# Optimization experiments

Hardware: AMD Instinct MI355X
Metric: run time of the kernel (lower is better)

## Reference

```python
import jax, jax.numpy as jnp
import numpy as np

HIDDEN = 1024
FFN = 4096
NUM_EXPERTS = 8
TOKENS = 4096


def setup_inputs() -> dict:
    key = jax.random.key(0)
    k1, k2, k3, k4 = jax.random.split(key, 4)
    x = jax.random.normal(k1, (TOKENS, HIDDEN), dtype=jnp.float32)
    router_weight = jax.random.normal(k2, (HIDDEN, NUM_EXPERTS), dtype=jnp.float32) * 0.02
    w1 = jax.random.normal(k3, (HIDDEN, FFN * NUM_EXPERTS), dtype=jnp.float32) * 0.02
    w2 = jax.random.normal(k4, (FFN * NUM_EXPERTS, HIDDEN), dtype=jnp.float32) * 0.02
    return {"x": x, "router_weight": router_weight, "w1": w1, "w2": w2, "top_k": 2}


def reference(x, router_weight, w1, w2, top_k):
    T, H = x.shape
    E = router_weight.shape[1]
    F = w1.shape[1] // E

    # Router: fp32 logits -> softmax -> top-k gating (sparse gates in dense [T, E] form)
    logits = x.astype(jnp.float32) @ router_weight  # [T, E]
    probs = jax.nn.softmax(logits, axis=-1)
    top_vals, top_idx = jax.lax.top_k(probs, top_k)  # [T, k]
    gates = jnp.zeros((T, E), dtype=probs.dtype).at[
        jnp.arange(T)[:, None], top_idx
    ].set(top_vals)  # [T, E], zero for non-selected experts

    # Per-expert FFN (expert-blocked weight layout: columns [e*F:(e+1)*F])
    w1e = w1.reshape(H, E, F)          # [H, E, F]
    w2e = w2.reshape(E, F, H)          # [E, F, H]
    h = jax.nn.gelu(jnp.einsum('th,hef->etf', x, w1e), approximate=False)  # [E, T, F]
    y = jnp.einsum('etf,efh->eth', h, w2e)  # [E, T, H]

    # Combine: gate-weighted sum over experts
    out = jnp.einsum('te,eth->th', gates.astype(y.dtype), y)  # [T, H]
    return out
```

## Files before the change

### kernel.cpp

```cpp
#include <hip/hip_runtime.h>
#include <hip/hip_bf16.h>

#define T_TOKENS 4096
#define HID 1024
#define FFN_ 4096
#define NE 8
#define MAXROWS 9216
#define MAXTILES 72

typedef unsigned short u16;
typedef __bf16 bf16x8 __attribute__((ext_vector_type(8)));
typedef float f32x4 __attribute__((ext_vector_type(4)));
typedef u16 u16x8 __attribute__((ext_vector_type(8)));

__device__ __forceinline__ u16 f2bf(float f) {
  __hip_bfloat16 h = __float2bfloat16(f);
  return *reinterpret_cast<u16*>(&h);
}

__device__ __forceinline__ void gload16(const void* g, void* l) {
  __builtin_amdgcn_global_load_lds(
      (const __attribute__((address_space(1))) void*)g,
      (__attribute__((address_space(3))) void*)l, 16, 0, 0);
}

__global__ __launch_bounds__(256) void router_kernel(
    const float* __restrict__ x, const float* __restrict__ rw,
    int* __restrict__ sel, float* __restrict__ gsel) {
  int token = blockIdx.x * 4 + (threadIdx.x >> 6);
  int lane = threadIdx.x & 63;
  const float* xr = x + (size_t)token * HID;
  float acc[8];
#pragma unroll
  for (int e = 0; e < 8; e++) acc[e] = 0.f;
  for (int h = lane; h < HID; h += 64) {
    float xv = xr[h];
    float4 r0 = *(const float4*)(rw + h * 8);
    float4 r1 = *(const float4*)(rw + h * 8 + 4);
    acc[0] += xv * r0.x; acc[1] += xv * r0.y; acc[2] += xv * r0.z; acc[3] += xv * r0.w;
    acc[4] += xv * r1.x; acc[5] += xv * r1.y; acc[6] += xv * r1.z; acc[7] += xv * r1.w;
  }
#pragma unroll
  for (int e = 0; e < 8; e++) {
#pragma unroll
    for (int o = 32; o > 0; o >>= 1) acc[e] += __shfl_down(acc[e], o);
  }
  if (lane == 0) {
    float mx = acc[0];
#pragma unroll
    for (int e = 1; e < 8; e++) mx = fmaxf(mx, acc[e]);
    float p[8], s = 0.f;
#pragma unroll
    for (int e = 0; e < 8; e++) { p[e] = expf(acc[e] - mx); s += p[e]; }
    float v0 = -1.f; int i0 = 0;
#pragma unroll
    for (int e = 0; e < 8; e++) if (p[e] > v0) { v0 = p[e]; i0 = e; }
    float v1 = -1.f; int i1 = 0;
#pragma unroll
    for (int e = 0; e < 8; e++) if (e != i0 && p[e] > v1) { v1 = p[e]; i1 = e; }
    float inv = 1.f / s;
    sel[token * 2] = i0;     gsel[token * 2] = v0 * inv;
    sel[token * 2 + 1] = i1; gsel[token * 2 + 1] = v1 * inv;
  }
}

__global__ __launch_bounds__(256) void hist_kernel(const int* __restrict__ sel,
                                                   int* __restrict__ counts) {
  __shared__ int lc[NE];
  if (threadIdx.x < NE) lc[threadIdx.x] = 0;
  __syncthreads();
  int p = blockIdx.x * 256 + threadIdx.x;
  atomicAdd(&lc[sel[p]], 1);
  __syncthreads();
  if (threadIdx.x < NE) atomicAdd(&counts[threadIdx.x], lc[threadIdx.x]);
}

__global__ void base_kernel(const int* __restrict__ counts, int* __restrict__ cursor,
                            int* __restrict__ tilemap) {
  if (threadIdx.x == 0) {
    int base = 0;
    for (int e = 0; e < NE; e++) {
      cursor[e] = base;
      int padded = (base + counts[e] + 127) & ~127;
      for (int t = base >> 7; t < (padded >> 7); t++) tilemap[t] = e;
      base = padded;
    }
    for (int t = base >> 7; t < MAXTILES; t++) tilemap[t] = 0;
  }
}

__global__ __launch_bounds__(256) void fill_kernel(int* __restrict__ perm,
                                                   float* __restrict__ grow) {
  int i = blockIdx.x * 256 + threadIdx.x;
  if (i < MAXROWS) { perm[i] = -1; grow[i] = 0.f; }
}

__global__ __launch_bounds__(256) void scatter_kernel(
    const int* __restrict__ sel, const float* __restrict__ gsel,
    int* __restrict__ cursor, int* __restrict__ perm, float* __restrict__ grow) {
  int p = blockIdx.x * 256 + threadIdx.x;
  int e = sel[p];
  int pos = atomicAdd(&cursor[e], 1);
  perm[pos] = p >> 1;
  grow[pos] = gsel[p];
}

__global__ __launch_bounds__(256) void convert_x(const float* __restrict__ x, u16* __restrict__ xb) {
  int i = (blockIdx.x * 256 + threadIdx.x) * 8;
  float4 a = *(const float4*)(x + i);
  float4 b = *(const float4*)(x + i + 4);
  u16x8 o;
  o[0] = f2bf(a.x); o[1] = f2bf(a.y); o[2] = f2bf(a.z); o[3] = f2bf(a.w);
  o[4] = f2bf(b.x); o[5] = f2bf(b.y); o[6] = f2bf(b.z); o[7] = f2bf(b.w);
  *(u16x8*)(xb + i) = o;
}

__global__ __launch_bounds__(256) void transpose_w1(const float* __restrict__ w1, u16* __restrict__ w1t) {
  __shared__ float tile[64][65];
  int c0 = blockIdx.x * 64;
  int r0 = blockIdx.y * 64;
  int t = threadIdx.x;
  int ci = (t & 15) * 4;
  int ri = t >> 4;
#pragma unroll
  for (int rr = 0; rr < 64; rr += 16) {
    float4 v = *(const float4*)(w1 + (size_t)(r0 + ri + rr) * 32768 + c0 + ci);
    tile[ri + rr][ci] = v.x; tile[ri + rr][ci + 1] = v.y;
    tile[ri + rr][ci + 2] = v.z; tile[ri + rr][ci + 3] = v.w;
  }
  __syncthreads();
  int j = t >> 2;
  int q = t & 3;
  u16x8 o0, o1;
#pragma unroll
  for (int k = 0; k < 8; k++) o0[k] = f2bf(tile[q * 16 + k][j]);
#pragma unroll
  for (int k = 0; k < 8; k++) o1[k] = f2bf(tile[q * 16 + 8 + k][j]);
  u16* dst = w1t + (size_t)(c0 + j) * 1024 + r0 + q * 16;
  *(u16x8*)dst = o0;
  *(u16x8*)(dst + 8) = o1;
}

__global__ __launch_bounds__(256) void transpose_w2(const float* __restrict__ w2, u16* __restrict__ w2t) {
  __shared__ float tile[64][65];
  int fb = blockIdx.x;
  int h0 = blockIdx.y * 64;
  int e = fb >> 6;
  int f0 = (fb & 63) * 64;
  int t = threadIdx.x;
  int ci = (t & 15) * 4;
  int ri = t >> 4;
#pragma unroll
  for (int rr = 0; rr < 64; rr += 16) {
    float4 v = *(const float4*)(w2 + (size_t)(fb * 64 + ri + rr) * 1024 + h0 + ci);
    tile[ri + rr][ci] = v.x; tile[ri + rr][ci + 1] = v.y;
    tile[ri + rr][ci + 2] = v.z; tile[ri + rr][ci + 3] = v.w;
  }
  __syncthreads();
  int j = t >> 2;
  int q = t & 3;
  u16x8 o0, o1;
#pragma unroll
  for (int k = 0; k < 8; k++) o0[k] = f2bf(tile[q * 16 + k][j]);
#pragma unroll
  for (int k = 0; k < 8; k++) o1[k] = f2bf(tile[q * 16 + 8 + k][j]);
  u16* dst = w2t + (size_t)e * 4194304 + (size_t)(h0 + j) * 4096 + f0 + q * 16;
  *(u16x8*)dst = o0;
  *(u16x8*)(dst + 8) = o1;
}

__global__ __launch_bounds__(256) void gemm1_kernel(
    const u16* __restrict__ xb, const u16* __restrict__ w1t,
    const int* __restrict__ perm, const float* __restrict__ grow,
    const int* __restrict__ tilemap, u16* __restrict__ hbuf,
    const u16* __restrict__ zp) {
  int mt = blockIdx.x, nt = blockIdx.y;
  int e = tilemap[mt];
  int row0 = mt * 128;
  int t = threadIdx.x, lane = t & 63, wave = t >> 6;
  __shared__ u16 As[128 * 64], Bs[128 * 64];

  const u16* asrc[4]; int astep[4];
  const u16* bsrc[4];
#pragma unroll
  for (int i = 0; i < 4; i++) {
    int chunk = i * 256 + t, row = chunk >> 3, c = chunk & 7;
    int cs = c ^ (row & 7);
    int tok = perm[row0 + row];
    if (tok >= 0) { asrc[i] = xb + (size_t)tok * 1024 + cs * 8; astep[i] = 64; }
    else { asrc[i] = zp + cs * 8; astep[i] = 0; }
    bsrc[i] = w1t + (size_t)e * 4194304 + (size_t)(nt * 128 + row) * 1024 + cs * 8;
  }

  f32x4 acc[4][4] = {};
  int wm = (wave >> 1) * 64, wn = (wave & 1) * 64;
  int r = lane & 15, kg = lane >> 4;

  for (int ks = 0; ks < 16; ks++) {
#pragma unroll
    for (int i = 0; i < 4; i++)
      gload16(asrc[i], (char*)As + i * 4096 + wave * 1024);
#pragma unroll
    for (int i = 0; i < 4; i++)
      gload16(bsrc[i], (char*)Bs + i * 4096 + wave * 1024);
    __syncthreads();
#pragma unroll
    for (int kk = 0; kk < 2; kk++) {
      bf16x8 af[4], bfr[4];
      int kb = kk * 64 + kg * 16;
#pragma unroll
      for (int mi = 0; mi < 4; mi++) {
        int rr = wm + mi * 16 + r;
        af[mi] = *(const bf16x8*)((const char*)As + rr * 128 + (kb ^ ((rr & 7) << 4)));
      }
#pragma unroll
      for (int ni = 0; ni < 4; ni++) {
        int rr = wn + ni * 16 + r;
        bfr[ni] = *(const bf16x8*)((const char*)Bs + rr * 128 + (kb ^ ((rr & 7) << 4)));
      }
#pragma unroll
      for (int mi = 0; mi < 4; mi++)
#pragma unroll
        for (int ni = 0; ni < 4; ni++)
          acc[mi][ni] = __builtin_amdgcn_mfma_f32_16x16x32_bf16(af[mi], bfr[ni], acc[mi][ni], 0, 0, 0);
    }
    __syncthreads();
#pragma unroll
    for (int i = 0; i < 4; i++) { asrc[i] += astep[i]; bsrc[i] += 64; }
  }

  float g[4][4];
#pragma unroll
  for (int mi = 0; mi < 4; mi++)
#pragma unroll
    for (int j = 0; j < 4; j++)
      g[mi][j] = grow[row0 + wm + mi * 16 + kg * 4 + j];
#pragma unroll
  for (int mi = 0; mi < 4; mi++)
#pragma unroll
    for (int ni = 0; ni < 4; ni++)
#pragma unroll
      for (int j = 0; j < 4; j++) {
        int rl = wm + mi * 16 + kg * 4 + j;
        int col = nt * 128 + wn + ni * 16 + r;
        float v = acc[mi][ni][j];
        float ge = 0.5f * v * (1.0f + erff(v * 0.7071067811865475f)) * g[mi][j];
        hbuf[(size_t)(row0 + rl) * 4096 + col] = f2bf(ge);
      }
}

__global__ __launch_bounds__(256) void gemm2_kernel(
    const u16* __restrict__ hbuf, const u16* __restrict__ w2t,
    const int* __restrict__ perm, const int* __restrict__ tilemap,
    float* __restrict__ out) {
  int mt = blockIdx.x, nt = blockIdx.y;
  int e = tilemap[mt];
  int row0 = mt * 128;
  int t = threadIdx.x, lane = t & 63, wave = t >> 6;
  __shared__ u16 As[128 * 64], Bs[128 * 64];

  const u16* asrc[4];
  const u16* bsrc[4];
#pragma unroll
  for (int i = 0; i < 4; i++) {
    int chunk = i * 256 + t, row = chunk >> 3, c = chunk & 7;
    int cs = c ^ (row & 7);
    asrc[i] = hbuf + (size_t)(row0 + row) * 4096 + cs * 8;
    bsrc[i] = w2t + (size_t)e * 4194304 + (size_t)(nt * 128 + row) * 4096 + cs * 8;
  }

  f32x4 acc[4][4] = {};
  int wm = (wave >> 1) * 64, wn = (wave & 1) * 64;
  int r = lane & 15, kg = lane >> 4;

  for (int ks = 0; ks < 64; ks++) {
#pragma unroll
    for (int i = 0; i < 4; i++)
      gload16(asrc[i], (char*)As + i * 4096 + wave * 1024);
#pragma unroll
    for (int i = 0; i < 4; i++)
      gload16(bsrc[i], (char*)Bs + i * 4096 + wave * 1024);
    __syncthreads();
#pragma unroll
    for (int kk = 0; kk < 2; kk++) {
      bf16x8 af[4], bfr[4];
      int kb = kk * 64 + kg * 16;
#pragma unroll
      for (int mi = 0; mi < 4; mi++) {
        int rr = wm + mi * 16 + r;
        af[mi] = *(const bf16x8*)((const char*)As + rr * 128 + (kb ^ ((rr & 7) << 4)));
      }
#pragma unroll
      for (int ni = 0; ni < 4; ni++) {
        int rr = wn + ni * 16 + r;
        bfr[ni] = *(const bf16x8*)((const char*)Bs + rr * 128 + (kb ^ ((rr & 7) << 4)));
      }
#pragma unroll
      for (int mi = 0; mi < 4; mi++)
#pragma unroll
        for (int ni = 0; ni < 4; ni++)
          acc[mi][ni] = __builtin_amdgcn_mfma_f32_16x16x32_bf16(af[mi], bfr[ni], acc[mi][ni], 0, 0, 0);
    }
    __syncthreads();
#pragma unroll
    for (int i = 0; i < 4; i++) { asrc[i] += 64; bsrc[i] += 64; }
  }

  int tok[4][4];
#pragma unroll
  for (int mi = 0; mi < 4; mi++)
#pragma unroll
    for (int j = 0; j < 4; j++)
      tok[mi][j] = perm[row0 + wm + mi * 16 + kg * 4 + j];
#pragma unroll
  for (int mi = 0; mi < 4; mi++)
#pragma unroll
    for (int ni = 0; ni < 4; ni++)
#pragma unroll
      for (int j = 0; j < 4; j++) {
        if (tok[mi][j] >= 0) {
          int col = nt * 128 + wn + ni * 16 + r;
          atomicAdd(out + (size_t)tok[mi][j] * 1024 + col, acc[mi][ni][j]);
        }
      }
}

extern "C" void kernel_launch(void* const* d_in, const int* in_sizes, int n_in,
                              void* d_out, int out_size, void* d_ws, size_t ws_size,
                              hipStream_t stream) {
  const float* x  = (const float*)d_in[0];
  const float* rw = (const float*)d_in[1];
  const float* w1 = (const float*)d_in[2];
  const float* w2 = (const float*)d_in[3];
  float* out = (float*)d_out;
  char* ws = (char*)d_ws;

  size_t off = 0;
  auto take = [&](size_t n) { char* p = ws + off; off += (n + 255) & ~255ull; return p; };
  u16* w1t   = (u16*)take(8ull * 4096 * 1024 * 2);
  u16* w2t   = (u16*)take(8ull * 4096 * 1024 * 2);
  u16* xb    = (u16*)take((size_t)T_TOKENS * HID * 2);
  u16* hbuf  = (u16*)take((size_t)MAXROWS * FFN_ * 2);
  int* sel   = (int*)take(T_TOKENS * 2 * 4);
  float* gsel = (float*)take(T_TOKENS * 2 * 4);
  int* perm  = (int*)take(MAXROWS * 4);
  float* grow = (float*)take(MAXROWS * 4);
  int* tmap  = (int*)take(MAXTILES * 4);
  int* counts = (int*)take(NE * 4);
  int* cursor = (int*)take(NE * 4);
  u16* zp    = (u16*)take(4096);

  hipMemsetAsync(zp, 0, 4096, stream);
  hipMemsetAsync(counts, 0, NE * 4, stream);
  hipMemsetAsync(out, 0, (size_t)T_TOKENS * HID * 4, stream);

  convert_x<<<dim3(T_TOKENS * HID / (256 * 8)), 256, 0, stream>>>(x, xb);
  transpose_w1<<<dim3(512, 16), 256, 0, stream>>>(w1, w1t);
  transpose_w2<<<dim3(512, 16), 256, 0, stream>>>(w2, w2t);
  router_kernel<<<dim3(T_TOKENS / 4), 256, 0, stream>>>(x, rw, sel, gsel);
  hist_kernel<<<dim3(T_TOKENS * 2 / 256), 256, 0, stream>>>(sel, counts);
  base_kernel<<<dim3(1), 64, 0, stream>>>(counts, cursor, tmap);
  fill_kernel<<<dim3((MAXROWS + 255) / 256), 256, 0, stream>>>(perm, grow);
  scatter_kernel<<<dim3(T_TOKENS * 2 / 256), 256, 0, stream>>>(sel, gsel, cursor, perm, grow);
  gemm1_kernel<<<dim3(MAXTILES, 32), 256, 0, stream>>>(xb, w1t, perm, grow, tmap, hbuf, zp);
  gemm2_kernel<<<dim3(MAXTILES, 8), 256, 0, stream>>>(hbuf, w2t, perm, tmap, out);
}
```

Before: 475.3 us.

## Pipeline expert GEMMs with triple-buffered LDS, larger tiles, split-K and XCD mapping

Both expert GEMMs move to 512-thread blocks with 256-row M tiles. They use a three-stage LDS ring filled by async global-to-LDS loads with explicit vmcnt waits, and raise wave priority around the MFMA blocks. gemm2 splits K four ways with atomic accumulation, and block IDs are remapped so M tiles stay on the same XCD for L2 reuse. The x-to-bf16 conversion is folded into the router, and the perm/grow fill is merged into the histogram kernel to cut launches. The trade-offs are higher padding waste with 256-row tiles, four times more atomics in gemm2, and a large LDS footprint that limits occupancy to one block.

```diff
diff --git a/kernel.cpp b/kernel.cpp
--- a/kernel.cpp
+++ b/kernel.cpp
@@ -5,8 +5,8 @@
 #define HID 1024
 #define FFN_ 4096
 #define NE 8
-#define MAXROWS 9216
-#define MAXTILES 72
+#define MAXROWS 10240
+#define MAXTILES 40
 
 typedef unsigned short u16;
 typedef __bf16 bf16x8 __attribute__((ext_vector_type(8)));
@@ -24,17 +24,23 @@
       (__attribute__((address_space(3))) void*)l, 16, 0, 0);
 }
 
+#define WAIT_VM6() asm volatile("s_waitcnt vmcnt(6)" ::: "memory")
+#define WAIT_VM0() asm volatile("s_waitcnt vmcnt(0)" ::: "memory")
+#define BARRIER()  asm volatile("s_barrier" ::: "memory")
+
 __global__ __launch_bounds__(256) void router_kernel(
     const float* __restrict__ x, const float* __restrict__ rw,
-    int* __restrict__ sel, float* __restrict__ gsel) {
+    int* __restrict__ sel, float* __restrict__ gsel, u16* __restrict__ xb) {
   int token = blockIdx.x * 4 + (threadIdx.x >> 6);
   int lane = threadIdx.x & 63;
   const float* xr = x + (size_t)token * HID;
+  u16* xbr = xb + (size_t)token * HID;
   float acc[8];
 #pragma unroll
   for (int e = 0; e < 8; e++) acc[e] = 0.f;
   for (int h = lane; h < HID; h += 64) {
     float xv = xr[h];
+    xbr[h] = f2bf(xv);
     float4 r0 = *(const float4*)(rw + h * 8);
     float4 r1 = *(const float4*)(rw + h * 8 + 4);
     acc[0] += xv * r0.x; acc[1] += xv * r0.y; acc[2] += xv * r0.z; acc[3] += xv * r0.w;
@@ -64,15 +70,18 @@
   }
 }
 
-__global__ __launch_bounds__(256) void hist_kernel(const int* __restrict__ sel,
-                                                   int* __restrict__ counts) {
+__global__ __launch_bounds__(256) void hist_fill_kernel(
+    const int* __restrict__ sel, int* __restrict__ counts,
+    int* __restrict__ perm, float* __restrict__ grow) {
   __shared__ int lc[NE];
   if (threadIdx.x < NE) lc[threadIdx.x] = 0;
   __syncthreads();
-  int p = blockIdx.x * 256 + threadIdx.x;
-  atomicAdd(&lc[sel[p]], 1);
+  int gid = blockIdx.x * 256 + threadIdx.x;
+  if (gid < T_TOKENS * 2) atomicAdd(&lc[sel[gid]], 1);
+  if (gid < MAXROWS) { perm[gid] = -1; grow[gid] = 0.f; }
   __syncthreads();
-  if (threadIdx.x < NE) atomicAdd(&counts[threadIdx.x], lc[threadIdx.x]);
+  if (threadIdx.x < NE && lc[threadIdx.x] > 0)
+    atomicAdd(&counts[threadIdx.x], lc[threadIdx.x]);
 }
 
 __global__ void base_kernel(const int* __restrict__ counts, int* __restrict__ cursor,
@@ -81,18 +90,12 @@
     int base = 0;
     for (int e = 0; e < NE; e++) {
       cursor[e] = base;
-      int padded = (base + counts[e] + 127) & ~127;
-      for (int t = base >> 7; t < (padded >> 7); t++) tilemap[t] = e;
+      int padded = (base + counts[e] + 255) & ~255;
+      for (int t = base >> 8; t < (padded >> 8); t++) tilemap[t] = e;
       base = padded;
     }
-    for (int t = base >> 7; t < MAXTILES; t++) tilemap[t] = 0;
-  }
-}
-
-__global__ __launch_bounds__(256) void fill_kernel(int* __restrict__ perm,
-                                                   float* __restrict__ grow) {
-  int i = blockIdx.x * 256 + threadIdx.x;
-  if (i < MAXROWS) { perm[i] = -1; grow[i] = 0.f; }
+    for (int t = base >> 8; t < MAXTILES; t++) tilemap[t] = 0;
+  }
 }
 
 __global__ __launch_bounds__(256) void scatter_kernel(
@@ -103,16 +106,6 @@
   int pos = atomicAdd(&cursor[e], 1);
   perm[pos] = p >> 1;
   grow[pos] = gsel[p];
-}
-
-__global__ __launch_bounds__(256) void convert_x(const float* __restrict__ x, u16* __restrict__ xb) {
-  int i = (blockIdx.x * 256 + threadIdx.x) * 8;
-  float4 a = *(const float4*)(x + i);
-  float4 b = *(const float4*)(x + i + 4);
-  u16x8 o;
-  o[0] = f2bf(a.x); o[1] = f2bf(a.y); o[2] = f2bf(a.z); o[3] = f2bf(a.w);
-  o[4] = f2bf(b.x); o[5] = f2bf(b.y); o[6] = f2bf(b.z); o[7] = f2bf(b.w);
-  *(u16x8*)(xb + i) = o;
 }
 
 __global__ __launch_bounds__(256) void transpose_w1(const float* __restrict__ w1, u16* __restrict__ w1t) {
@@ -169,64 +162,87 @@
   *(u16x8*)(dst + 8) = o1;
 }
 
-__global__ __launch_bounds__(256) void gemm1_kernel(
+__global__ __launch_bounds__(512, 1) void gemm1_kernel(
     const u16* __restrict__ xb, const u16* __restrict__ w1t,
     const int* __restrict__ perm, const float* __restrict__ grow,
     const int* __restrict__ tilemap, u16* __restrict__ hbuf,
     const u16* __restrict__ zp) {
-  int mt = blockIdx.x, nt = blockIdx.y;
+  int bid = blockIdx.x;
+  int xcd = bid & 7, pos = bid >> 3;
+  int nt = pos / 5;
+  int mt = xcd * 5 + (pos - nt * 5);
   int e = tilemap[mt];
-  int row0 = mt * 128;
+  int row0 = mt * 256;
   int t = threadIdx.x, lane = t & 63, wave = t >> 6;
-  __shared__ u16 As[128 * 64], Bs[128 * 64];
+  __shared__ u16 As[3][256 * 64], Bs[3][128 * 64];
 
   const u16* asrc[4]; int astep[4];
-  const u16* bsrc[4];
+  const u16* bsrc[2];
 #pragma unroll
   for (int i = 0; i < 4; i++) {
-    int chunk = i * 256 + t, row = chunk >> 3, c = chunk & 7;
+    int chunk = i * 512 + t, row = chunk >> 3, c = chunk & 7;
     int cs = c ^ (row & 7);
     int tok = perm[row0 + row];
     if (tok >= 0) { asrc[i] = xb + (size_t)tok * 1024 + cs * 8; astep[i] = 64; }
     else { asrc[i] = zp + cs * 8; astep[i] = 0; }
+  }
+#pragma unroll
+  for (int i = 0; i < 2; i++) {
+    int chunk = i * 512 + t, row = chunk >> 3, c = chunk & 7;
+    int cs = c ^ (row & 7);
     bsrc[i] = w1t + (size_t)e * 4194304 + (size_t)(nt * 128 + row) * 1024 + cs * 8;
   }
 
   f32x4 acc[4][4] = {};
-  int wm = (wave >> 1) * 64, wn = (wave & 1) * 64;
+  int wm = wave >> 1, wn = wave & 1;
   int r = lane & 15, kg = lane >> 4;
 
-  for (int ks = 0; ks < 16; ks++) {
+  auto stage = [&](int s) {
 #pragma unroll
     for (int i = 0; i < 4; i++)
-      gload16(asrc[i], (char*)As + i * 4096 + wave * 1024);
-#pragma unroll
-    for (int i = 0; i < 4; i++)
-      gload16(bsrc[i], (char*)Bs + i * 4096 + wave * 1024);
-    __syncthreads();
+      gload16(asrc[i], (char*)&As[s][0] + i * 8192 + wave * 1024);
+#pragma unroll
+    for (int i = 0; i < 2; i++)
+      gload16(bsrc[i], (char*)&Bs[s][0] + i * 8192 + wave * 1024);
+#pragma unroll
+    for (int i = 0; i < 4; i++) asrc[i] += astep[i];
+#pragma unroll
+    for (int i = 0; i < 2; i++) bsrc[i] += 64;
+  };
+  auto compute = [&](int s) {
+    const char* Ab = (const char*)&As[s][0];
+    const char* Bb = (const char*)&Bs[s][0];
 #pragma unroll
     for (int kk = 0; kk < 2; kk++) {
+      int kb = kk * 64 + kg * 16;
       bf16x8 af[4], bfr[4];
-      int kb = kk * 64 + kg * 16;
 #pragma unroll
       for (int mi = 0; mi < 4; mi++) {
-        int rr = wm + mi * 16 + r;
-        af[mi] = *(const bf16x8*)((const char*)As + rr * 128 + (kb ^ ((rr & 7) << 4)));
+        int rr = wm * 64 + mi * 16 + r;
+        af[mi] = *(const bf16x8*)(Ab + rr * 128 + (kb ^ ((rr & 7) << 4)));
       }
 #pragma unroll
       for (int ni = 0; ni < 4; ni++) {
-        int rr = wn + ni * 16 + r;
-        bfr[ni] = *(const bf16x8*)((const char*)Bs + rr * 128 + (kb ^ ((rr & 7) << 4)));
-      }
+        int rr = wn * 64 + ni * 16 + r;
+        bfr[ni] = *(const bf16x8*)(Bb + rr * 128 + (kb ^ ((rr & 7) << 4)));
+      }
+      __builtin_amdgcn_s_setprio(1);
 #pragma unroll
       for (int mi = 0; mi < 4; mi++)
 #pragma unroll
         for (int ni = 0; ni < 4; ni++)
           acc[mi][ni] = __builtin_amdgcn_mfma_f32_16x16x32_bf16(af[mi], bfr[ni], acc[mi][ni], 0, 0, 0);
+      __builtin_amdgcn_s_setprio(0);
     }
-    __syncthreads();
-#pragma unroll
-    for (int i = 0; i < 4; i++) { asrc[i] += astep[i]; bsrc[i] += 64; }
+  };
+
+  stage(0);
+  stage(1);
+  for (int kt = 0; kt < 16; kt++) {
+    if (kt == 15) { WAIT_VM0(); } else { WAIT_VM6(); }
+    BARRIER();
+    compute(kt % 3);
+    if (kt < 14) stage((kt + 2) % 3);
   }
 
   float g[4][4];
@@ -234,76 +250,101 @@
   for (int mi = 0; mi < 4; mi++)
 #pragma unroll
     for (int j = 0; j < 4; j++)
-      g[mi][j] = grow[row0 + wm + mi * 16 + kg * 4 + j];
+      g[mi][j] = grow[row0 + wm * 64 + mi * 16 + kg * 4 + j];
 #pragma unroll
   for (int mi = 0; mi < 4; mi++)
 #pragma unroll
     for (int ni = 0; ni < 4; ni++)
 #pragma unroll
       for (int j = 0; j < 4; j++) {
-        int rl = wm + mi * 16 + kg * 4 + j;
-        int col = nt * 128 + wn + ni * 16 + r;
+        int rl = wm * 64 + mi * 16 + kg * 4 + j;
+        int col = nt * 128 + wn * 64 + ni * 16 + r;
         float v = acc[mi][ni][j];
         float ge = 0.5f * v * (1.0f + erff(v * 0.7071067811865475f)) * g[mi][j];
         hbuf[(size_t)(row0 + rl) * 4096 + col] = f2bf(ge);
       }
 }
 
-__global__ __launch_bounds__(256) void gemm2_kernel(
+__global__ __launch_bounds__(512, 1) void gemm2_kernel(
     const u16* __restrict__ hbuf, const u16* __restrict__ w2t,
     const int* __restrict__ perm, const int* __restrict__ tilemap,
     float* __restrict__ out) {
-  int mt = blockIdx.x, nt = blockIdx.y;
+  int bid = blockIdx.x;
+  int xcd = bid & 7, pos = bid >> 3;
+  int c32 = pos / 5;
+  int mt = xcd * 5 + (pos - c32 * 5);
+  int ksp = c32 >> 3;
+  int nt = c32 & 7;
   int e = tilemap[mt];
-  int row0 = mt * 128;
+  int row0 = mt * 256;
   int t = threadIdx.x, lane = t & 63, wave = t >> 6;
-  __shared__ u16 As[128 * 64], Bs[128 * 64];
+  __shared__ u16 As[3][256 * 64], Bs[3][128 * 64];
 
   const u16* asrc[4];
-  const u16* bsrc[4];
+  const u16* bsrc[2];
 #pragma unroll
   for (int i = 0; i < 4; i++) {
-    int chunk = i * 256 + t, row = chunk >> 3, c = chunk & 7;
+    int chunk = i * 512 + t, row = chunk >> 3, c = chunk & 7;
     int cs = c ^ (row & 7);
-    asrc[i] = hbuf + (size_t)(row0 + row) * 4096 + cs * 8;
-    bsrc[i] = w2t + (size_t)e * 4194304 + (size_t)(nt * 128 + row) * 4096 + cs * 8;
+    asrc[i] = hbuf + (size_t)(row0 + row) * 4096 + (size_t)ksp * 1024 + cs * 8;
+  }
+#pragma unroll
+  for (int i = 0; i < 2; i++) {
+    int chunk = i * 512 + t, row = chunk >> 3, c = chunk & 7;
+    int cs = c ^ (row & 7);
+    bsrc[i] = w2t + (size_t)e * 4194304 + (size_t)(nt * 128 + row) * 4096 + (size_t)ksp * 1024 + cs * 8;
   }
 
   f32x4 acc[4][4] = {};
-  int wm = (wave >> 1) * 64, wn = (wave & 1) * 64;
+  int wm = wave >> 1, wn = wave & 1;
   int r = lane & 15, kg = lane >> 4;
 
-  for (int ks = 0; ks < 64; ks++) {
+  auto stage = [&](int s) {
 #pragma unroll
     for (int i = 0; i < 4; i++)
-      gload16(asrc[i], (char*)As + i * 4096 + wave * 1024);
-#pragma unroll
-    for (int i = 0; i < 4; i++)
-      gload16(bsrc[i], (char*)Bs + i * 4096 + wave * 1024);
-    __syncthreads();
+      gload16(asrc[i], (char*)&As[s][0] + i * 8192 + wave * 1024);
+#pragma unroll
+    for (int i = 0; i < 2; i++)
+      gload16(bsrc[i], (char*)&Bs[s][0] + i * 8192 + wave * 1024);
+#pragma unroll
+    for (int i = 0; i < 4; i++) asrc[i] += 64;
+#pragma unroll
+    for (int i = 0; i < 2; i++) bsrc[i] += 64;
+  };
+  auto compute = [&](int s) {
+    const char* Ab = (const char*)&As[s][0];
+    const char* Bb = (const char*)&Bs[s][0];
 #pragma unroll
     for (int kk = 0; kk < 2; kk++) {
+      int kb = kk * 64 + kg * 16;
       bf16x8 af[4], bfr[4];
-      int kb = kk * 64 + kg * 16;
 #pragma unroll
       for (int mi = 0; mi < 4; mi++) {
-        int rr = wm + mi * 16 + r;
-        af[mi] = *(const bf16x8*)((const char*)As + rr * 128 + (kb ^ ((rr & 7) << 4)));
+        int rr = wm * 64 + mi * 16 + r;
+        af[mi] = *(const bf16x8*)(Ab + rr * 128 + (kb ^ ((rr & 7) << 4)));
       }
 #pragma unroll
       for (int ni = 0; ni < 4; ni++) {
-        int rr = wn + ni * 16 + r;
-        bfr[ni] = *(const bf16x8*)((const char*)Bs + rr * 128 + (kb ^ ((rr & 7) << 4)));
-      }
+        int rr = wn * 64 + ni * 16 + r;
+        bfr[ni] = *(const bf16x8*)(Bb + rr * 128 + (kb ^ ((rr & 7) << 4)));
+      }
+      __builtin_amdgcn_s_setprio(1);
 #pragma unroll
       for (int mi = 0; mi < 4; mi++)
 #pragma unroll
         for (int ni = 0; ni < 4; ni++)
           acc[mi][ni] = __builtin_amdgcn_mfma_f32_16x16x32_bf16(af[mi], bfr[ni], acc[mi][ni], 0, 0, 0);
+      __builtin_amdgcn_s_setprio(0);
     }
-    __syncthreads();
-#pragma unroll
-    for (int i = 0; i < 4; i++) { asrc[i] += 64; bsrc[i] += 64; }
+  };
+
+  stage(0);
+  stage(1);
+  for (int kt = 0; kt < 16; kt++) {
+    if (kt == 15) { WAIT_VM0(); } else { WAIT_VM6(); }
+    BARRIER();
+    compute(kt % 3);
+    if (kt < 14) stage((kt + 2) % 3);
   }
 
   int tok[4][4];
@@ -311,7 +352,7 @@
   for (int mi = 0; mi < 4; mi++)
 #pragma unroll
     for (int j = 0; j < 4; j++)
-      tok[mi][j] = perm[row0 + wm + mi * 16 + kg * 4 + j];
+      tok[mi][j] = perm[row0 + wm * 64 + mi * 16 + kg * 4 + j];
 #pragma unroll
   for (int mi = 0; mi < 4; mi++)
 #pragma unroll
@@ -319,7 +360,7 @@
 #pragma unroll
       for (int j = 0; j < 4; j++) {
         if (tok[mi][j] >= 0) {
-          int col = nt * 128 + wn + ni * 16 + r;
+          int col = nt * 128 + wn * 64 + ni * 16 + r;
           atomicAdd(out + (size_t)tok[mi][j] * 1024 + col, acc[mi][ni][j]);
         }
       }
@@ -354,14 +395,12 @@
   hipMemsetAsync(counts, 0, NE * 4, stream);
   hipMemsetAsync(out, 0, (size_t)T_TOKENS * HID * 4, stream);
 
-  convert_x<<<dim3(T_TOKENS * HID / (256 * 8)), 256, 0, stream>>>(x, xb);
   transpose_w1<<<dim3(512, 16), 256, 0, stream>>>(w1, w1t);
   transpose_w2<<<dim3(512, 16), 256, 0, stream>>>(w2, w2t);
-  router_kernel<<<dim3(T_TOKENS / 4), 256, 0, stream>>>(x, rw, sel, gsel);
-  hist_kernel<<<dim3(T_TOKENS * 2 / 256), 256, 0, stream>>>(sel, counts);
+  router_kernel<<<dim3(T_TOKENS / 4), 256, 0, stream>>>(x, rw, sel, gsel, xb);
+  hist_fill_kernel<<<dim3(MAXROWS / 256), 256, 0, stream>>>(sel, counts, perm, grow);
   base_kernel<<<dim3(1), 64, 0, stream>>>(counts, cursor, tmap);
-  fill_kernel<<<dim3((MAXROWS + 255) / 256), 256, 0, stream>>>(perm, grow);
   scatter_kernel<<<dim3(T_TOKENS * 2 / 256), 256, 0, stream>>>(sel, gsel, cursor, perm, grow);
-  gemm1_kernel<<<dim3(MAXTILES, 32), 256, 0, stream>>>(xb, w1t, perm, grow, tmap, hbuf, zp);
-  gemm2_kernel<<<dim3(MAXTILES, 8), 256, 0, stream>>>(hbuf, w2t, perm, tmap, out);
-}
+  gemm1_kernel<<<dim3(1280), 512, 0, stream>>>(xb, w1t, perm, grow, tmap, hbuf, zp);
+  gemm2_kernel<<<dim3(1280), 512, 0, stream>>>(hbuf, w2t, perm, tmap, out);
+}
```

Result: faster. 440.4 us (-7.3%).
